# Kernel optimization log

Measured on AMD Instinct MI355X. Metric: run time of the kernel, lower is better.

The kernel has to match this reference:

```python
import jax, jax.numpy as jnp
from jax import lax
import numpy as np

VOCAB = 50257
EMB = 768
HID = [1024, 1024, 1024]
B, S = 2, 2048
LN_EPS_RNN = 1e-5   # torch default inside MinGRU layers
LN_EPS_OUT = 0.0    # NLPModel passes bias=False into LayerNorm's eps slot


def _layernorm(x, w, b, eps):
    mu = jnp.mean(x, axis=-1, keepdims=True)
    var = jnp.var(x, axis=-1, keepdims=True)
    return (x - mu) * lax.rsqrt(var + eps) * w + b


def _log_g(x):
    # log of g(x) = where(x>=0, x+0.5, sigmoid(x)), computed stably in log space
    return jnp.where(x >= 0, jnp.log(jax.nn.relu(x) + 0.5), -jax.nn.softplus(-x))


def _mingru_scan(gate, hidden, h0):
    # gate, hidden: [B,S,H]; h0: [B,1,H] (positive). Log-space parallel scan.
    log_coeffs = -jax.nn.softplus(gate)              # log(1-z)
    log_values = -jax.nn.softplus(-gate) + _log_g(hidden)  # log(z) + log g(h~)
    log_coeffs = jnp.pad(log_coeffs, ((0, 0), (1, 0), (0, 0)))
    log_values = jnp.concatenate([jnp.log(h0), log_values], axis=1)
    a_star = jnp.cumsum(log_coeffs, axis=1)
    log_h = a_star + lax.cumlogsumexp(log_values - a_star, axis=1)
    return jnp.exp(log_h)[:, 1:]                     # [B,S,H]


def setup_inputs() -> dict:
    key = jax.random.key(0)
    ks = jax.random.split(key, 8)
    inp = {}
    inp["ids"] = jax.random.randint(ks[0], (B, S), 0, VOCAB)
    inp["emb_W"] = jax.random.normal(ks[1], (VOCAB, EMB)) * 0.02
    dims = [EMB] + HID
    for l, (i, o) in enumerate(zip(dims[:-1], dims[1:])):
        inp[f"ln{l}_w"] = jnp.ones((i,))
        inp[f"ln{l}_b"] = jnp.zeros((i,))
        inp[f"gates{l}_W"] = jax.random.normal(jax.random.fold_in(key, 10 + l), (2 * o, i)) * (1.0 / np.sqrt(i))
    inp["res0_W"] = jax.random.normal(ks[2], (HID[0], EMB)) * (1.0 / np.sqrt(EMB))
    inp["lnf_w"] = jnp.ones((HID[-1],))
    inp["lnf_b"] = jnp.zeros((HID[-1],))
    inp["fc_W"] = jax.random.normal(ks[3], (VOCAB, HID[-1])) * 0.02
    inp["fc_b"] = jnp.zeros((VOCAB,))
    return inp


def reference(ids, emb_W, ln0_w, ln0_b, gates0_W, res0_W,
              ln1_w, ln1_b, gates1_W, ln2_w, ln2_b, gates2_W,
              lnf_w, lnf_b, fc_W, fc_b):
    x = emb_W[ids]                                   # [B,S,EMB]
    layers = [
        (ln0_w, ln0_b, gates0_W, res0_W),
        (ln1_w, ln1_b, gates1_W, None),
        (ln2_w, ln2_b, gates2_W, None),
    ]
    inp = x
    for ln_w, ln_b, gW, resW in layers:
        out_dim = gW.shape[0] // 2
        xn = _layernorm(inp, ln_w, ln_b, LN_EPS_RNN)
        gh = jnp.einsum('bsi,oi->bso', xn, gW)       # bias=False for minGRU
        gate, hidden = jnp.split(gh, 2, axis=-1)
        h0 = jnp.full((inp.shape[0], 1, out_dim), 0.5, dtype=inp.dtype)  # g(0)=0.5
        out = _mingru_scan(gate, hidden, h0)
        res = inp if resW is None else jnp.einsum('bsi,oi->bso', inp, resW)
        inp = out + res                              # residual, dropout=0
    x = _layernorm(inp, lnf_w, lnf_b, LN_EPS_OUT)
    logits = jnp.einsum('bsh,vh->bsv', x, fc_W) + fc_b
    return logits
```

## Files before the change

### kernel.cpp

```cpp
#include <hip/hip_runtime.h>
#include <stdint.h>
#include <stddef.h>


typedef __attribute__((ext_vector_type(4))) float f32x4;
typedef __attribute__((ext_vector_type(8))) short bf16x8;
typedef float f32x4u __attribute__((vector_size(16), aligned(4)));

__device__ __forceinline__ unsigned short f2bf(float f) {
  unsigned int u = __float_as_uint(f);
  u += 0x7FFFu + ((u >> 16) & 1u);
  return (unsigned short)(u >> 16);
}

__device__ __forceinline__ void gload16(const void* g, void* l) {
  __builtin_amdgcn_global_load_lds(
      (const __attribute__((address_space(1))) void*)g,
      (__attribute__((address_space(3))) void*)l, 16, 0, 0);
}

#define MEMFENCE asm volatile("" ::: "memory")

__global__ __launch_bounds__(256) void cvt_kernel(
    const float* __restrict__ in, unsigned short* __restrict__ out, int n8) {
  int i = blockIdx.x * 256 + threadIdx.x;
  int stride = gridDim.x * 256;
  for (; i < n8; i += stride) {
    const float4* p = (const float4*)in + (size_t)i * 2;
    float4 a = p[0], b = p[1];
    bf16x8 o;
    o[0] = (short)f2bf(a.x); o[1] = (short)f2bf(a.y);
    o[2] = (short)f2bf(a.z); o[3] = (short)f2bf(a.w);
    o[4] = (short)f2bf(b.x); o[5] = (short)f2bf(b.y);
    o[6] = (short)f2bf(b.z); o[7] = (short)f2bf(b.w);
    *(bf16x8*)(out + (size_t)i * 8) = o;
  }
}

__global__ __launch_bounds__(256) void embed_kernel(
    const int* __restrict__ ids, const float* __restrict__ embW,
    unsigned short* __restrict__ xbf) {
  int tok = blockIdx.x;
  int id = ids[tok];
  const float* src = embW + (size_t)id * 768;
  unsigned short* dst = xbf + (size_t)tok * 768;
  for (int j = threadIdx.x; j < 768; j += 256) dst[j] = f2bf(src[j]);
}

template <int BF16IN, int D>
__global__ __launch_bounds__(256) void ln_kernel(
    const void* __restrict__ xin, const float* __restrict__ w,
    const float* __restrict__ b, unsigned short* __restrict__ xout,
    float eps) {
  constexpr int NV = D / 256;
  int row = blockIdx.x;
  int tid = threadIdx.x;
  int lane = tid & 63, wid = tid >> 6;
  const float* xf = (const float*)xin;
  const unsigned short* xb = (const unsigned short*)xin;
  float vals[NV];
  float s = 0.f, ss = 0.f;
#pragma unroll
  for (int i = 0; i < NV; i++) {
    size_t idx = (size_t)row * D + i * 256 + tid;
    float v;
    if (BF16IN) {
      unsigned int u = ((unsigned int)xb[idx]) << 16;
      v = __uint_as_float(u);
    } else {
      v = xf[idx];
    }
    vals[i] = v;
    s += v;
    ss += v * v;
  }
  for (int off = 32; off; off >>= 1) {
    s += __shfl_down(s, off);
    ss += __shfl_down(ss, off);
  }
  __shared__ float red[8];
  if (lane == 0) { red[wid] = s; red[4 + wid] = ss; }
  __syncthreads();
  s = red[0] + red[1] + red[2] + red[3];
  ss = red[4] + red[5] + red[6] + red[7];
  constexpr float invD = 1.f / (float)D;
  float mu = s * invD;
  float var = ss * invD - mu * mu;
  float inv = rsqrtf(var + eps);
#pragma unroll
  for (int i = 0; i < NV; i++) {
    int col = i * 256 + tid;
    size_t idx = (size_t)row * D + col;
    float y = (vals[i] - mu) * inv * w[col] + b[col];
    xout[idx] = f2bf(y);
  }
}

__global__ __launch_bounds__(256) void gemm_bt(
    const unsigned short* __restrict__ A, const unsigned short* __restrict__ B,
    float* __restrict__ C, int M, int N, int K) {
  __shared__ __align__(16) char smem[16896];
  unsigned short* lsA = (unsigned short*)smem;
  unsigned short* lsB = (unsigned short*)(smem + 8192);
  float* lsC = (float*)smem;

  const int tid = threadIdx.x;
  const int lane = tid & 63;
  const int wid = __builtin_amdgcn_readfirstlane(tid >> 6);
  const int row0 = blockIdx.y * 128;
  const int col0 = blockIdx.x * 128;

  const int srow = tid >> 2;
  const int skg = (tid & 3) * 8;

  const unsigned short* gA0 = A + (size_t)(row0 + srow) * K + skg;
  const unsigned short* gA1 = A + (size_t)(row0 + 64 + srow) * K + skg;
  const unsigned short* gB0 = B + (size_t)(col0 + srow) * K + skg;
  const unsigned short* gB1 = B + (size_t)(col0 + 64 + srow) * K + skg;

  char* ldsA0 = (char*)lsA + wid * 1024;
  char* ldsA1 = (char*)lsA + 4096 + wid * 1024;
  char* ldsB0 = (char*)lsB + wid * 1024;
  char* ldsB1 = (char*)lsB + 4096 + wid * 1024;

  const int wm = wid >> 1, wn = wid & 1;
  const unsigned short* pA = lsA + (wm * 64 + (lane & 15)) * 32 + (lane >> 4) * 8;
  const unsigned short* pB = lsB + (wn * 64 + (lane & 15)) * 32 + (lane >> 4) * 8;

  f32x4 acc[4][4] = {};

  for (int k0 = 0; k0 < K; k0 += 32) {
    gload16(gA0 + k0, ldsA0);
    gload16(gA1 + k0, ldsA1);
    gload16(gB0 + k0, ldsB0);
    gload16(gB1 + k0, ldsB1);
    __syncthreads();
    bf16x8 af[4], bfr[4];
#pragma unroll
    for (int i = 0; i < 4; i++) af[i] = *(const bf16x8*)(pA + i * 512);
#pragma unroll
    for (int i = 0; i < 4; i++) bfr[i] = *(const bf16x8*)(pB + i * 512);
#pragma unroll
    for (int i = 0; i < 4; i++)
#pragma unroll
      for (int j = 0; j < 4; j++)
        acc[i][j] = __builtin_amdgcn_mfma_f32_16x16x32_bf16(bfr[j], af[i],
                                                            acc[i][j], 0, 0, 0);
    __syncthreads();
  }

  const int mloc = lane & 15;
  const int ng = (lane >> 4) * 4;
  const int LDC = 132;
  const int trow = tid >> 5;
  const int tcol = (tid & 31) * 4;
#pragma unroll
  for (int c = 0; c < 4; c++) {
    if (wm == (c >> 1)) {
      const int i0 = 2 * (c & 1);
#pragma unroll
      for (int ii = 0; ii < 2; ii++)
#pragma unroll
        for (int j = 0; j < 4; j++)
          *(f32x4*)(lsC + (ii * 16 + mloc) * LDC + wn * 64 + j * 16 + ng) =
              acc[i0 + ii][j];
    }
    __syncthreads();
#pragma unroll
    for (int rr = 0; rr < 4; rr++) {
      const int r = rr * 8 + trow;
      const size_t gr = row0 + c * 32 + r;
      f32x4 v = *(const f32x4*)(lsC + r * LDC + tcol);
      *(f32x4*)(C + gr * N + col0 + tcol) = v;
    }
    __syncthreads();
  }
}

__global__ __launch_bounds__(256) void gemm_final64(
    const unsigned short* __restrict__ A, const unsigned short* __restrict__ B,
    float* __restrict__ C, const float* __restrict__ bias, int M, int N,
    int K) {
  __shared__ __align__(16) char smem[65536];
  float* const lsC = (float*)smem;

  const int t = threadIdx.x;
  const int l = t & 63;
  const int w = __builtin_amdgcn_readfirstlane(t >> 6);
  const int row0 = blockIdx.x * 128;
  const int col0 = blockIdx.y * 128;

  const int srow = t >> 3;
  const int sg = ((t & 7) ^ (srow & 7)) * 8;
  const unsigned short* gA0 = A + (size_t)(row0 + srow) * K + sg;
  const unsigned short* gA1 = A + (size_t)(row0 + 32 + srow) * K + sg;
  const unsigned short* gA2 = A + (size_t)(row0 + 64 + srow) * K + sg;
  const unsigned short* gA3 = A + (size_t)(row0 + 96 + srow) * K + sg;
  int b0 = min(col0 + srow, N - 1);
  int b1 = min(col0 + 32 + srow, N - 1);
  int b2 = min(col0 + 64 + srow, N - 1);
  int b3 = min(col0 + 96 + srow, N - 1);
  const unsigned short* gB0 = B + (size_t)b0 * K + sg;
  const unsigned short* gB1 = B + (size_t)b1 * K + sg;
  const unsigned short* gB2 = B + (size_t)b2 * K + sg;
  const unsigned short* gB3 = B + (size_t)b3 * K + sg;
  const int wOff = w * 1024;

  const int wm = w >> 1, wn = w & 1;
  const int aRowB = (wm * 64 + (l & 15)) * 128;
  const int bRowB = (wn * 64 + (l & 15)) * 128;
  const int gk0 = (((l >> 4)) ^ (l & 7)) * 16;
  const int gk1 = ((4 + (l >> 4)) ^ (l & 7)) * 16;

  f32x4 acc[4][4] = {};

#define STAGE(BUF, KOFF)                            \
  do {                                              \
    char* a_ = smem + (BUF) * 32768;                \
    char* b_ = a_ + 16384;                          \
    gload16(gA0 + (KOFF), a_ + wOff);               \
    gload16(gA1 + (KOFF), a_ + 4096 + wOff);        \
    gload16(gA2 + (KOFF), a_ + 8192 + wOff);        \
    gload16(gA3 + (KOFF), a_ + 12288 + wOff);       \
    gload16(gB0 + (KOFF), b_ + wOff);               \
    gload16(gB1 + (KOFF), b_ + 4096 + wOff);        \
    gload16(gB2 + (KOFF), b_ + 8192 + wOff);        \
    gload16(gB3 + (KOFF), b_ + 12288 + wOff);       \
  } while (0)

  STAGE(0, 0);

  const int NK = K >> 6;
  for (int kt = 0; kt < NK; ++kt) {
    const int cur = kt & 1;
    const char* aB = smem + cur * 32768;
    const char* bB = aB + 16384;

    if (kt + 1 < NK) {
      STAGE(cur ^ 1, (kt + 1) << 6);
      asm volatile("s_waitcnt vmcnt(8)" ::: "memory");
    } else {
      asm volatile("s_waitcnt vmcnt(0)" ::: "memory");
    }
    __builtin_amdgcn_s_barrier();
    MEMFENCE;

    bf16x8 af[4][2], bfr[4][2];
#pragma unroll
    for (int i = 0; i < 4; i++) {
      af[i][0] = *(const bf16x8*)(aB + aRowB + i * 2048 + gk0);
      af[i][1] = *(const bf16x8*)(aB + aRowB + i * 2048 + gk1);
    }
#pragma unroll
    for (int j = 0; j < 4; j++) {
      bfr[j][0] = *(const bf16x8*)(bB + bRowB + j * 2048 + gk0);
      bfr[j][1] = *(const bf16x8*)(bB + bRowB + j * 2048 + gk1);
    }
#pragma unroll
    for (int i = 0; i < 4; i++)
#pragma unroll
      for (int j = 0; j < 4; j++) {
        acc[i][j] = __builtin_amdgcn_mfma_f32_16x16x32_bf16(
            bfr[j][0], af[i][0], acc[i][j], 0, 0, 0);
        acc[i][j] = __builtin_amdgcn_mfma_f32_16x16x32_bf16(
            bfr[j][1], af[i][1], acc[i][j], 0, 0, 0);
      }

    MEMFENCE;
    __builtin_amdgcn_s_barrier();
    MEMFENCE;
  }
#undef STAGE

  const int mloc = l & 15;
  const int ng = (l >> 4) * 4;
  const int LDC = 132;
  const int trow = t >> 5;
  const int tcol = (t & 31) * 4;
#pragma unroll
  for (int c = 0; c < 4; c++) {
    if (wm == (c >> 1)) {
      const int i0 = 2 * (c & 1);
#pragma unroll
      for (int ii = 0; ii < 2; ii++)
#pragma unroll
        for (int j = 0; j < 4; j++)
          *(f32x4*)(lsC + (ii * 16 + mloc) * LDC + wn * 64 + j * 16 + ng) =
              acc[i0 + ii][j];
    }
    __syncthreads();
#pragma unroll
    for (int rr = 0; rr < 4; rr++) {
      const int r = rr * 8 + trow;
      const size_t gr = row0 + c * 32 + r;
      f32x4 v = *(const f32x4*)(lsC + r * LDC + tcol);
      const int n0 = col0 + tcol;
      if (col0 + 128 <= N) {
        const f32x4u bv = *(const f32x4u*)(bias + n0);
        f32x4u o;
#pragma unroll
        for (int q = 0; q < 4; q++) o[q] = v[q] + bv[q];
        __builtin_nontemporal_store(o, (f32x4u*)(C + gr * N + n0));
      } else {
#pragma unroll
        for (int q = 0; q < 4; q++)
          if (n0 + q < N) C[gr * N + n0 + q] = v[q] + bias[n0 + q];
      }
    }
    __syncthreads();
  }
}

__device__ __forceinline__ void gru_step(float gate, float hid, float& a,
                                         float& g) {
  a = 1.f / (1.f + expf(gate));
  g = (hid >= 0.f) ? (hid + 0.5f) : 1.f / (1.f + expf(-hid));
}

__global__ __launch_bounds__(256) void scan_compose(
    const float* __restrict__ gh, float* __restrict__ Acl,
    float* __restrict__ Vcl) {
  int ck = blockIdx.x;
  int hp = blockIdx.y * 256 + threadIdx.x;
  int b = hp >> 10, h = hp & 1023;
  const float* gb = gh + ((size_t)(b * 2048 + ck * 64)) * 2048 + h;
  float A = 1.f, V = 0.f;
  for (int t = 0; t < 64; t++) {
    float gate = gb[(size_t)t * 2048];
    float hid = gb[(size_t)t * 2048 + 1024];
    float a, g;
    gru_step(gate, hid, a, g);
    V = a * V + (1.f - a) * g;
    A *= a;
  }
  size_t i = (size_t)(b * 32 + ck) * 1024 + h;
  Acl[i] = A;
  Vcl[i] = V;
}

__global__ __launch_bounds__(256) void scan_prefix(
    const float* __restrict__ Acl, const float* __restrict__ Vcl,
    float* __restrict__ Hin) {
  int hp = blockIdx.x * 256 + threadIdx.x;
  int b = hp >> 10, h = hp & 1023;
  float hr = 0.5f;
  for (int ck = 0; ck < 32; ck++) {
    size_t i = (size_t)(b * 32 + ck) * 1024 + h;
    Hin[i] = hr;
    hr = Acl[i] * hr + Vcl[i];
  }
}

__global__ __launch_bounds__(256) void scan_emit(
    const float* __restrict__ gh, const float* __restrict__ Hin,
    const float* __restrict__ res, float* __restrict__ xout) {
  int ck = blockIdx.x;
  int hp = blockIdx.y * 256 + threadIdx.x;
  int b = hp >> 10, h = hp & 1023;
  const float* gb = gh + ((size_t)(b * 2048 + ck * 64)) * 2048 + h;
  const float* rb = res + ((size_t)(b * 2048 + ck * 64)) * 1024 + h;
  float* ob = xout + ((size_t)(b * 2048 + ck * 64)) * 1024 + h;
  float hc = Hin[(size_t)(b * 32 + ck) * 1024 + h];
  for (int t = 0; t < 64; t++) {
    float gate = gb[(size_t)t * 2048];
    float hid = gb[(size_t)t * 2048 + 1024];
    float a, g;
    gru_step(gate, hid, a, g);
    hc = a * hc + (1.f - a) * g;
    ob[(size_t)t * 1024] = hc + rb[(size_t)t * 1024];
  }
}

extern "C" void kernel_launch(void* const* d_in, const int* in_sizes, int n_in,
                              void* d_out, int out_size, void* d_ws,
                              size_t ws_size, hipStream_t stream) {
  (void)in_sizes; (void)n_in; (void)out_size; (void)ws_size;
  const int* ids = (const int*)d_in[0];
  const float* embW = (const float*)d_in[1];
  const float* ln0w = (const float*)d_in[2];
  const float* ln0b = (const float*)d_in[3];
  const float* g0W = (const float*)d_in[4];
  const float* ln1w = (const float*)d_in[5];
  const float* ln1b = (const float*)d_in[6];
  const float* g1W = (const float*)d_in[7];
  const float* ln2w = (const float*)d_in[8];
  const float* ln2b = (const float*)d_in[9];
  const float* g2W = (const float*)d_in[10];
  const float* r0W = (const float*)d_in[11];
  const float* lnfw = (const float*)d_in[12];
  const float* lnfb = (const float*)d_in[13];
  const float* fcW = (const float*)d_in[14];
  const float* fcb = (const float*)d_in[15];
  float* out = (float*)d_out;

  const int M = 4096;
  const int V = 50257;

  char* ws = (char*)d_ws;
  unsigned short* x_bf = (unsigned short*)(ws + 0);
  float* x_f = (float*)(ws + 6291456);
  unsigned short* xn_bf = (unsigned short*)(ws + 23068672);
  float* gh = (float*)(ws + 31457280);
  float* r0 = (float*)(ws + 65011712);
  float* Acl = (float*)(ws + 81788928);
  float* Vcl = (float*)(ws + 82051072);
  float* Hin = (float*)(ws + 82313216);
  unsigned short* gwbf = (unsigned short*)(ws + 82575360);
  unsigned short* rwbf = (unsigned short*)(ws + 86769664);
  unsigned short* fcwbf = (unsigned short*)(ws + 88342528);

  auto cvt = [&](const float* src, unsigned short* dst, int n) {
    int n8 = n / 8;
    int grid = min((n8 + 255) / 256, 2048);
    cvt_kernel<<<grid, 256, 0, stream>>>(src, dst, n8);
  };

  embed_kernel<<<M, 256, 0, stream>>>(ids, embW, x_bf);
  cvt(fcW, fcwbf, V * 1024);
  cvt(r0W, rwbf, 1024 * 768);

  cvt(g0W, gwbf, 2048 * 768);
  ln_kernel<1, 768><<<M, 256, 0, stream>>>(x_bf, ln0w, ln0b, xn_bf, 1e-5f);
  gemm_bt<<<dim3(16, 32), 256, 0, stream>>>(xn_bf, gwbf, gh, M, 2048, 768);
  gemm_bt<<<dim3(8, 32), 256, 0, stream>>>(x_bf, rwbf, r0, M, 1024, 768);
  scan_compose<<<dim3(32, 8), 256, 0, stream>>>(gh, Acl, Vcl);
  scan_prefix<<<8, 256, 0, stream>>>(Acl, Vcl, Hin);
  scan_emit<<<dim3(32, 8), 256, 0, stream>>>(gh, Hin, r0, x_f);

  cvt(g1W, gwbf, 2048 * 1024);
  ln_kernel<0, 1024><<<M, 256, 0, stream>>>(x_f, ln1w, ln1b, xn_bf, 1e-5f);
  gemm_bt<<<dim3(16, 32), 256, 0, stream>>>(xn_bf, gwbf, gh, M, 2048, 1024);
  scan_compose<<<dim3(32, 8), 256, 0, stream>>>(gh, Acl, Vcl);
  scan_prefix<<<8, 256, 0, stream>>>(Acl, Vcl, Hin);
  scan_emit<<<dim3(32, 8), 256, 0, stream>>>(gh, Hin, x_f, x_f);

  cvt(g2W, gwbf, 2048 * 1024);
  ln_kernel<0, 1024><<<M, 256, 0, stream>>>(x_f, ln2w, ln2b, xn_bf, 1e-5f);
  gemm_bt<<<dim3(16, 32), 256, 0, stream>>>(xn_bf, gwbf, gh, M, 2048, 1024);
  scan_compose<<<dim3(32, 8), 256, 0, stream>>>(gh, Acl, Vcl);
  scan_prefix<<<8, 256, 0, stream>>>(Acl, Vcl, Hin);
  scan_emit<<<dim3(32, 8), 256, 0, stream>>>(gh, Hin, x_f, x_f);

  ln_kernel<0, 1024><<<M, 256, 0, stream>>>(x_f, lnfw, lnfb, xn_bf, 0.0f);
  gemm_final64<<<dim3(32, (V + 127) / 128), 256, 0, stream>>>(
      xn_bf, fcwbf, out, fcb, M, V, 1024);
}
```

Before: 900.9 us.

## Enlarge final vocab GEMM tile to 256x256 with 512-thread blocks

The final logits GEMM moves from 128x128 tiles with 256 threads to 256x256 tiles with 512 threads (8 waves, each computing 128x64). Shared memory doubles to 128KB for double-buffered A/B staging, and the epilogue writes eight 32-row chunks. The goal is more operand reuse per byte loaded and fewer blocks over the huge vocabulary dimension. In exchange, register pressure rises from the 8x4 accumulators, occupancy drops to one block per CU, and there is more padding waste on the last column tile.

```diff
diff --git a/kernel.cpp b/kernel.cpp
--- a/kernel.cpp
+++ b/kernel.cpp
@@ -177,55 +177,55 @@
   }
 }
 
-__global__ __launch_bounds__(256) void gemm_final64(
+__global__ __launch_bounds__(512) void gemm_final256(
     const unsigned short* __restrict__ A, const unsigned short* __restrict__ B,
     float* __restrict__ C, const float* __restrict__ bias, int M, int N,
     int K) {
-  __shared__ __align__(16) char smem[65536];
+  __shared__ __align__(16) char smem[131072];
   float* const lsC = (float*)smem;
 
   const int t = threadIdx.x;
   const int l = t & 63;
   const int w = __builtin_amdgcn_readfirstlane(t >> 6);
-  const int row0 = blockIdx.x * 128;
-  const int col0 = blockIdx.y * 128;
+  const int row0 = blockIdx.x * 256;
+  const int col0 = blockIdx.y * 256;
 
   const int srow = t >> 3;
   const int sg = ((t & 7) ^ (srow & 7)) * 8;
-  const unsigned short* gA0 = A + (size_t)(row0 + srow) * K + sg;
-  const unsigned short* gA1 = A + (size_t)(row0 + 32 + srow) * K + sg;
-  const unsigned short* gA2 = A + (size_t)(row0 + 64 + srow) * K + sg;
-  const unsigned short* gA3 = A + (size_t)(row0 + 96 + srow) * K + sg;
+  const unsigned short* aS0 = A + (size_t)(row0 + srow) * K + sg;
+  const unsigned short* aS1 = A + (size_t)(row0 + 64 + srow) * K + sg;
+  const unsigned short* aS2 = A + (size_t)(row0 + 128 + srow) * K + sg;
+  const unsigned short* aS3 = A + (size_t)(row0 + 192 + srow) * K + sg;
   int b0 = min(col0 + srow, N - 1);
-  int b1 = min(col0 + 32 + srow, N - 1);
-  int b2 = min(col0 + 64 + srow, N - 1);
-  int b3 = min(col0 + 96 + srow, N - 1);
-  const unsigned short* gB0 = B + (size_t)b0 * K + sg;
-  const unsigned short* gB1 = B + (size_t)b1 * K + sg;
-  const unsigned short* gB2 = B + (size_t)b2 * K + sg;
-  const unsigned short* gB3 = B + (size_t)b3 * K + sg;
+  int b1 = min(col0 + 64 + srow, N - 1);
+  int b2 = min(col0 + 128 + srow, N - 1);
+  int b3 = min(col0 + 192 + srow, N - 1);
+  const unsigned short* bS0 = B + (size_t)b0 * K + sg;
+  const unsigned short* bS1 = B + (size_t)b1 * K + sg;
+  const unsigned short* bS2 = B + (size_t)b2 * K + sg;
+  const unsigned short* bS3 = B + (size_t)b3 * K + sg;
   const int wOff = w * 1024;
 
-  const int wm = w >> 1, wn = w & 1;
-  const int aRowB = (wm * 64 + (l & 15)) * 128;
+  const int wm = w >> 2, wn = w & 3;
+  const int aRowB = (wm * 128 + (l & 15)) * 128;
   const int bRowB = (wn * 64 + (l & 15)) * 128;
-  const int gk0 = (((l >> 4)) ^ (l & 7)) * 16;
+  const int gk0 = ((l >> 4) ^ (l & 7)) * 16;
   const int gk1 = ((4 + (l >> 4)) ^ (l & 7)) * 16;
 
-  f32x4 acc[4][4] = {};
-
-#define STAGE(BUF, KOFF)                            \
-  do {                                              \
-    char* a_ = smem + (BUF) * 32768;                \
-    char* b_ = a_ + 16384;                          \
-    gload16(gA0 + (KOFF), a_ + wOff);               \
-    gload16(gA1 + (KOFF), a_ + 4096 + wOff);        \
-    gload16(gA2 + (KOFF), a_ + 8192 + wOff);        \
-    gload16(gA3 + (KOFF), a_ + 12288 + wOff);       \
-    gload16(gB0 + (KOFF), b_ + wOff);               \
-    gload16(gB1 + (KOFF), b_ + 4096 + wOff);        \
-    gload16(gB2 + (KOFF), b_ + 8192 + wOff);        \
-    gload16(gB3 + (KOFF), b_ + 12288 + wOff);       \
+  f32x4 acc[8][4] = {};
+
+#define STAGE(BUF, KOFF)                       \
+  do {                                         \
+    char* a_ = smem + (BUF) * 65536;           \
+    char* b_ = a_ + 32768;                     \
+    gload16(aS0 + (KOFF), a_ + wOff);          \
+    gload16(aS1 + (KOFF), a_ + 8192 + wOff);   \
+    gload16(aS2 + (KOFF), a_ + 16384 + wOff);  \
+    gload16(aS3 + (KOFF), a_ + 24576 + wOff);  \
+    gload16(bS0 + (KOFF), b_ + wOff);          \
+    gload16(bS1 + (KOFF), b_ + 8192 + wOff);   \
+    gload16(bS2 + (KOFF), b_ + 16384 + wOff);  \
+    gload16(bS3 + (KOFF), b_ + 24576 + wOff);  \
   } while (0)
 
   STAGE(0, 0);
@@ -233,8 +233,8 @@
   const int NK = K >> 6;
   for (int kt = 0; kt < NK; ++kt) {
     const int cur = kt & 1;
-    const char* aB = smem + cur * 32768;
-    const char* bB = aB + 16384;
+    const char* aB = smem + cur * 65536;
+    const char* bB = aB + 32768;
 
     if (kt + 1 < NK) {
       STAGE(cur ^ 1, (kt + 1) << 6);
@@ -245,26 +245,30 @@
     __builtin_amdgcn_s_barrier();
     MEMFENCE;
 
-    bf16x8 af[4][2], bfr[4][2];
-#pragma unroll
-    for (int i = 0; i < 4; i++) {
-      af[i][0] = *(const bf16x8*)(aB + aRowB + i * 2048 + gk0);
-      af[i][1] = *(const bf16x8*)(aB + aRowB + i * 2048 + gk1);
-    }
+    bf16x8 bf[4][2];
 #pragma unroll
     for (int j = 0; j < 4; j++) {
-      bfr[j][0] = *(const bf16x8*)(bB + bRowB + j * 2048 + gk0);
-      bfr[j][1] = *(const bf16x8*)(bB + bRowB + j * 2048 + gk1);
-    }
-#pragma unroll
-    for (int i = 0; i < 4; i++)
-#pragma unroll
-      for (int j = 0; j < 4; j++) {
-        acc[i][j] = __builtin_amdgcn_mfma_f32_16x16x32_bf16(
-            bfr[j][0], af[i][0], acc[i][j], 0, 0, 0);
-        acc[i][j] = __builtin_amdgcn_mfma_f32_16x16x32_bf16(
-            bfr[j][1], af[i][1], acc[i][j], 0, 0, 0);
+      bf[j][0] = *(const bf16x8*)(bB + bRowB + j * 2048 + gk0);
+      bf[j][1] = *(const bf16x8*)(bB + bRowB + j * 2048 + gk1);
+    }
+#pragma unroll
+    for (int h = 0; h < 2; h++) {
+      bf16x8 af[4][2];
+#pragma unroll
+      for (int i = 0; i < 4; i++) {
+        af[i][0] = *(const bf16x8*)(aB + aRowB + (h * 4 + i) * 2048 + gk0);
+        af[i][1] = *(const bf16x8*)(aB + aRowB + (h * 4 + i) * 2048 + gk1);
       }
+#pragma unroll
+      for (int i = 0; i < 4; i++)
+#pragma unroll
+        for (int j = 0; j < 4; j++) {
+          acc[h * 4 + i][j] = __builtin_amdgcn_mfma_f32_16x16x32_bf16(
+              bf[j][0], af[i][0], acc[h * 4 + i][j], 0, 0, 0);
+          acc[h * 4 + i][j] = __builtin_amdgcn_mfma_f32_16x16x32_bf16(
+              bf[j][1], af[i][1], acc[h * 4 + i][j], 0, 0, 0);
+        }
+    }
 
     MEMFENCE;
     __builtin_amdgcn_s_barrier();
@@ -274,28 +278,26 @@
 
   const int mloc = l & 15;
   const int ng = (l >> 4) * 4;
-  const int LDC = 132;
-  const int trow = t >> 5;
-  const int tcol = (t & 31) * 4;
-#pragma unroll
-  for (int c = 0; c < 4; c++) {
-    if (wm == (c >> 1)) {
-      const int i0 = 2 * (c & 1);
+  const int LDC = 264;
+#pragma unroll
+  for (int c = 0; c < 8; c++) {
+    if (wm == (c >> 2)) {
+      const int fr0 = (c & 3) * 2;
 #pragma unroll
       for (int ii = 0; ii < 2; ii++)
 #pragma unroll
         for (int j = 0; j < 4; j++)
           *(f32x4*)(lsC + (ii * 16 + mloc) * LDC + wn * 64 + j * 16 + ng) =
-              acc[i0 + ii][j];
+              acc[fr0 + ii][j];
     }
     __syncthreads();
 #pragma unroll
     for (int rr = 0; rr < 4; rr++) {
-      const int r = rr * 8 + trow;
+      const int r = rr * 8 + (t >> 6);
       const size_t gr = row0 + c * 32 + r;
-      f32x4 v = *(const f32x4*)(lsC + r * LDC + tcol);
-      const int n0 = col0 + tcol;
-      if (col0 + 128 <= N) {
+      f32x4 v = *(const f32x4*)(lsC + r * LDC + (t & 63) * 4);
+      const int n0 = col0 + (t & 63) * 4;
+      if (col0 + 256 <= N) {
         const f32x4u bv = *(const f32x4u*)(bias + n0);
         f32x4u o;
 #pragma unroll
@@ -442,6 +444,6 @@
   scan_emit<<<dim3(32, 8), 256, 0, stream>>>(gh, Hin, x_f, x_f);
 
   ln_kernel<0, 1024><<<M, 256, 0, stream>>>(x_f, lnfw, lnfb, xn_bf, 0.0f);
-  gemm_final64<<<dim3(32, (V + 127) / 128), 256, 0, stream>>>(
+  gemm_final256<<<dim3(16, (V + 255) / 256), 512, 0, stream>>>(
       xn_bf, fcwbf, out, fcb, M, V, 1024);
 }
```

After: 905.6 us. No clear change (+0.5%).
